# Optimization experiments

Hardware: AMD Instinct MI355X
Metric: run time of the kernel (lower is better)

## Reference

```python
import jax, jax.numpy as jnp
import numpy as np

C = 8192          # class_num == batch (required by the original per-row loop)
LS = 0.1          # label_smooth
SKIP = 3          # skip_num


def setup_inputs() -> dict:
    key = jax.random.key(0)
    preds = jax.random.normal(key, (C, C), dtype=jnp.float32)
    targets = jnp.arange(C, dtype=jnp.int32)  # row i's gt class is i, matching the loop
    return {"preds": preds, "targets": targets}


def reference(preds, targets):
    n = preds.shape[1]
    logprobs = jax.nn.log_softmax(preds, axis=1)                     # [C, C]
    onehot = jax.nn.one_hot(targets, n, dtype=jnp.float32)
    # torch.clamp(one_hot, min=LS/(C-1), max=1-LS): label smoothing
    smoothed = jnp.clip(onehot, LS / (n - 1), 1.0 - LS)

    # Per row i, skip the top SKIP classes by logprob, skipping over the gt class i.
    # Taking top (SKIP+1) always contains enough non-gt entries.
    _, topk_idx = jax.lax.top_k(logprobs, SKIP + 1)                  # [C, SKIP+1]
    rows = jnp.arange(n)[:, None]
    is_gt = topk_idx == rows                                         # gt class in top-k?
    kept = ~is_gt
    rank = jnp.cumsum(kept.astype(jnp.int32), axis=1)                # 1-based rank among non-gt
    selected = kept & (rank <= SKIP)                                 # first SKIP non-gt entries

    # Scatter selected top-k indices into a [C, C] boolean skip mask.
    skip_mask = jnp.zeros((n, n), dtype=bool).at[rows, topk_idx].max(selected)

    # Row loss: -sum over non-skipped classes of smoothed_target * logprob.
    loss = -jnp.sum(jnp.where(skip_mask, 0.0, smoothed * logprobs), axis=1)  # [C]
    return jnp.mean(loss)
```

## Files before the change

### kernel.cpp

```cpp
#include <hip/hip_runtime.h>

#define C_DIM 8192
#define BLOCK 256
#define PER_THREAD 32
#define NVEC 8

__device__ __forceinline__ bool better(float a, int ia, float b, int ib) {
    return (a > b) || (a == b && ia < ib);
}

__device__ __forceinline__ void insert4(float v[4], int id[4], float x, int j) {
    if (better(x, j, v[3], id[3])) {
        v[3] = x; id[3] = j;
        if (better(v[3], id[3], v[2], id[2])) { float tv = v[2]; int ti = id[2]; v[2] = v[3]; id[2] = id[3]; v[3] = tv; id[3] = ti; }
        if (better(v[2], id[2], v[1], id[1])) { float tv = v[1]; int ti = id[1]; v[1] = v[2]; id[1] = id[2]; v[2] = tv; id[2] = ti; }
        if (better(v[1], id[1], v[0], id[0])) { float tv = v[0]; int ti = id[0]; v[0] = v[1]; id[0] = id[1]; v[1] = tv; id[1] = ti; }
    }
}

__device__ __forceinline__ int slot2col(int tid, int s) {
    return ((s >> 2) * BLOCK + tid) * 4 + (s & 3);
}

__global__ __launch_bounds__(BLOCK) void row_loss_kernel(const float* __restrict__ preds,
                                                         const int* __restrict__ targets,
                                                         float* __restrict__ row_loss) {
    const int row  = blockIdx.x;
    const int tid  = threadIdx.x;
    const int lane = tid & 63;
    const int wid  = tid >> 6;

    const float*  base = preds + (size_t)row * C_DIM;
    const float4* rp   = (const float4*)base;

    __shared__ float s_s[4], s_l[4];
    __shared__ float s_tv[16];
    __shared__ int   s_ti[16];

    float xgt = 0.0f;
    if (tid == 0) xgt = base[targets[row]];

    float r[PER_THREAD];
    float lsum = 0.0f;
    float lv = -INFINITY;
    int   ls = 0;

#pragma unroll
    for (int v = 0; v < NVEC; ++v) {
        float4 f = rp[v * BLOCK + tid];
        float e0 = f.x, e1 = f.y, e2 = f.z, e3 = f.w;
        r[v * 4 + 0] = e0; r[v * 4 + 1] = e1; r[v * 4 + 2] = e2; r[v * 4 + 3] = e3;
        lsum += (e0 + e1) + (e2 + e3);
        if (e0 > lv) { lv = e0; ls = v * 4 + 0; }
        if (e1 > lv) { lv = e1; ls = v * 4 + 1; }
        if (e2 > lv) { lv = e2; ls = v * 4 + 2; }
        if (e3 > lv) { lv = e3; ls = v * 4 + 3; }
    }

    float wsum = lsum;
#pragma unroll
    for (int o = 32; o; o >>= 1) wsum += __shfl_xor(wsum, o);
    if (lane == 0) s_s[wid] = wsum;

    int lj = slot2col(tid, ls);
    float wtv[4]; int wti[4];
#pragma unroll
    for (int round = 0; round < 4; ++round) {
        float rv = lv; int ri = lj;
#pragma unroll
        for (int o = 32; o; o >>= 1) {
            float ov = __shfl_xor(rv, o);
            int   oi = __shfl_xor(ri, o);
            if (better(ov, oi, rv, ri)) { rv = ov; ri = oi; }
        }
        wtv[round] = rv; wti[round] = ri;
        if (lj == ri) {
            r[ls] = -INFINITY;
            lv = r[0]; ls = 0;
#pragma unroll
            for (int k = 1; k < PER_THREAD; ++k)
                if (r[k] > lv) { lv = r[k]; ls = k; }
            lj = slot2col(tid, ls);
        }
    }
    if (lane == 0) {
#pragma unroll
        for (int k = 0; k < 4; ++k) { s_tv[wid * 4 + k] = wtv[k]; s_ti[wid * 4 + k] = wti[k]; }
    }
    __syncthreads();

    const float m = fmaxf(fmaxf(s_tv[0], s_tv[4]), fmaxf(s_tv[8], s_tv[12]));

    float le = 0.0f;
#pragma unroll
    for (int k = 0; k < PER_THREAD; ++k) le += __expf(r[k] - m);
#pragma unroll
    for (int o = 32; o; o >>= 1) le += __shfl_xor(le, o);
    if (lane == 0) s_l[wid] = le;
    __syncthreads();

    if (tid == 0) {
        const float Sx = s_s[0] + s_s[1] + s_s[2] + s_s[3];
        float l = s_l[0] + s_l[1] + s_l[2] + s_l[3];
#pragma unroll
        for (int k = 0; k < 16; ++k) l += __expf(s_tv[k] - m);

        float fv[4] = { -INFINITY, -INFINITY, -INFINITY, -INFINITY };
        int   fi[4] = { 0x7FFFFFFF, 0x7FFFFFFF, 0x7FFFFFFF, 0x7FFFFFFF };
#pragma unroll
        for (int k = 0; k < 16; ++k) insert4(fv, fi, s_tv[k], s_ti[k]);

        const float logZ  = m + __logf(l);
        const float lp_gt = xgt - logZ;

        float skip_x = 0.0f; int cnt = 0;
#pragma unroll
        for (int k = 0; k < 4; ++k)
            if (fi[k] != row && cnt < 3) { skip_x += fv[k]; ++cnt; }

        const float S_lp    = Sx - (float)C_DIM * logZ;
        const float skip_lp = skip_x - 3.0f * logZ;
        const float eps     = 0.1f / (float)(C_DIM - 1);

        row_loss[row] = -(0.9f * lp_gt + eps * (S_lp - lp_gt - skip_lp));
    }
}

__global__ __launch_bounds__(BLOCK) void mean_reduce_kernel(const float* __restrict__ row_loss,
                                                            float* __restrict__ out) {
    const int tid = threadIdx.x;
    float s = 0.0f;
    for (int i = tid; i < C_DIM; i += BLOCK) s += row_loss[i];
#pragma unroll
    for (int o = 32; o; o >>= 1) s += __shfl_xor(s, o);
    __shared__ float sm[4];
    if ((tid & 63) == 0) sm[tid >> 6] = s;
    __syncthreads();
    if (tid == 0) out[0] = (sm[0] + sm[1] + sm[2] + sm[3]) / (float)C_DIM;
}

extern "C" void kernel_launch(void* const* d_in, const int* in_sizes, int n_in,
                              void* d_out, int out_size, void* d_ws, size_t ws_size,
                              hipStream_t stream) {
    const float* preds   = (const float*)d_in[0];
    const int*   targets = (const int*)d_in[1];
    float*       out     = (float*)d_out;
    float*       ws      = (float*)d_ws;

    row_loss_kernel<<<C_DIM, BLOCK, 0, stream>>>(preds, targets, ws);
    mean_reduce_kernel<<<1, BLOCK, 0, stream>>>(ws, out);
}
```

Baseline: 371.7 us.

## Fuse exp-sum into load pass, drop max-shift and second barrier, simplify top-k

Each row's sum of exponentials is now accumulated in the same pass that loads the row, without subtracting the row max first. That removes the second exp loop, its warp reduction and one block-wide barrier. The per-warp top-4 selection now finds the max with fmaxf shuffles and uses a ballot to pick the owning lane, which recovers the column, instead of shuffling value/index pairs with tie-breaking. The mean reduction switches to float4 loads. Skipping the max shift risks exp overflow for large logits, and tie handling among equal values changes.

```diff
diff --git a/kernel.cpp b/kernel.cpp
--- a/kernel.cpp
+++ b/kernel.cpp
@@ -5,21 +5,13 @@
 #define PER_THREAD 32
 #define NVEC 8
 
-__device__ __forceinline__ bool better(float a, int ia, float b, int ib) {
-    return (a > b) || (a == b && ia < ib);
-}
-
 __device__ __forceinline__ void insert4(float v[4], int id[4], float x, int j) {
-    if (better(x, j, v[3], id[3])) {
+    if (x > v[3]) {
         v[3] = x; id[3] = j;
-        if (better(v[3], id[3], v[2], id[2])) { float tv = v[2]; int ti = id[2]; v[2] = v[3]; id[2] = id[3]; v[3] = tv; id[3] = ti; }
-        if (better(v[2], id[2], v[1], id[1])) { float tv = v[1]; int ti = id[1]; v[1] = v[2]; id[1] = id[2]; v[2] = tv; id[2] = ti; }
-        if (better(v[1], id[1], v[0], id[0])) { float tv = v[0]; int ti = id[0]; v[0] = v[1]; id[0] = id[1]; v[1] = tv; id[1] = ti; }
+        if (v[3] > v[2]) { float tv = v[2]; int ti = id[2]; v[2] = v[3]; id[2] = id[3]; v[3] = tv; id[3] = ti; }
+        if (v[2] > v[1]) { float tv = v[1]; int ti = id[1]; v[1] = v[2]; id[1] = id[2]; v[2] = tv; id[2] = ti; }
+        if (v[1] > v[0]) { float tv = v[0]; int ti = id[0]; v[0] = v[1]; id[0] = id[1]; v[1] = tv; id[1] = ti; }
     }
-}
-
-__device__ __forceinline__ int slot2col(int tid, int s) {
-    return ((s >> 2) * BLOCK + tid) * 4 + (s & 3);
 }
 
 __global__ __launch_bounds__(BLOCK) void row_loss_kernel(const float* __restrict__ preds,
@@ -41,76 +33,72 @@
     if (tid == 0) xgt = base[targets[row]];
 
     float r[PER_THREAD];
-    float lsum = 0.0f;
+    float lsum = 0.0f, lexp = 0.0f;
     float lv = -INFINITY;
-    int   ls = 0;
 
 #pragma unroll
     for (int v = 0; v < NVEC; ++v) {
         float4 f = rp[v * BLOCK + tid];
-        float e0 = f.x, e1 = f.y, e2 = f.z, e3 = f.w;
-        r[v * 4 + 0] = e0; r[v * 4 + 1] = e1; r[v * 4 + 2] = e2; r[v * 4 + 3] = e3;
-        lsum += (e0 + e1) + (e2 + e3);
-        if (e0 > lv) { lv = e0; ls = v * 4 + 0; }
-        if (e1 > lv) { lv = e1; ls = v * 4 + 1; }
-        if (e2 > lv) { lv = e2; ls = v * 4 + 2; }
-        if (e3 > lv) { lv = e3; ls = v * 4 + 3; }
+        r[v * 4 + 0] = f.x; r[v * 4 + 1] = f.y; r[v * 4 + 2] = f.z; r[v * 4 + 3] = f.w;
+        lsum += (f.x + f.y) + (f.z + f.w);
+        lexp += (__expf(f.x) + __expf(f.y)) + (__expf(f.z) + __expf(f.w));
+        lv = fmaxf(fmaxf(lv, fmaxf(f.x, f.y)), fmaxf(f.z, f.w));
     }
 
-    float wsum = lsum;
+    float wsum = lsum, wexp = lexp;
 #pragma unroll
-    for (int o = 32; o; o >>= 1) wsum += __shfl_xor(wsum, o);
-    if (lane == 0) s_s[wid] = wsum;
+    for (int o = 32; o; o >>= 1) {
+        wsum += __shfl_xor(wsum, o);
+        wexp += __shfl_xor(wexp, o);
+    }
 
-    int lj = slot2col(tid, ls);
     float wtv[4]; int wti[4];
 #pragma unroll
     for (int round = 0; round < 4; ++round) {
-        float rv = lv; int ri = lj;
+        float rv = lv;
 #pragma unroll
-        for (int o = 32; o; o >>= 1) {
-            float ov = __shfl_xor(rv, o);
-            int   oi = __shfl_xor(ri, o);
-            if (better(ov, oi, rv, ri)) { rv = ov; ri = oi; }
+        for (int o = 32; o; o >>= 1) rv = fmaxf(rv, __shfl_xor(rv, o));
+        unsigned long long own = __ballot(lv == rv);
+        int owner = __ffsll((long long)own) - 1;
+        int gcol = 0;
+        if (lane == owner) {
+            bool killed = false;
+            int slot = 0;
+#pragma unroll
+            for (int k = 0; k < PER_THREAD; ++k) {
+                bool hit = (!killed) && (r[k] == rv);
+                if (hit) { slot = k; killed = true; }
+            }
+#pragma unroll
+            for (int k = 0; k < PER_THREAD; ++k)
+                if (k == slot) r[k] = -INFINITY;
+            gcol = ((slot >> 2) * BLOCK + tid) * 4 + (slot & 3);
+            lv = r[0];
+#pragma unroll
+            for (int k = 1; k < PER_THREAD; ++k) lv = fmaxf(lv, r[k]);
         }
-        wtv[round] = rv; wti[round] = ri;
-        if (lj == ri) {
-            r[ls] = -INFINITY;
-            lv = r[0]; ls = 0;
-#pragma unroll
-            for (int k = 1; k < PER_THREAD; ++k)
-                if (r[k] > lv) { lv = r[k]; ls = k; }
-            lj = slot2col(tid, ls);
-        }
+        gcol = __shfl(gcol, owner);
+        wtv[round] = rv; wti[round] = gcol;
     }
+
     if (lane == 0) {
+        s_s[wid] = wsum;
+        s_l[wid] = wexp;
 #pragma unroll
         for (int k = 0; k < 4; ++k) { s_tv[wid * 4 + k] = wtv[k]; s_ti[wid * 4 + k] = wti[k]; }
     }
     __syncthreads();
 
-    const float m = fmaxf(fmaxf(s_tv[0], s_tv[4]), fmaxf(s_tv[8], s_tv[12]));
-
-    float le = 0.0f;
-#pragma unroll
-    for (int k = 0; k < PER_THREAD; ++k) le += __expf(r[k] - m);
-#pragma unroll
-    for (int o = 32; o; o >>= 1) le += __shfl_xor(le, o);
-    if (lane == 0) s_l[wid] = le;
-    __syncthreads();
-
     if (tid == 0) {
-        const float Sx = s_s[0] + s_s[1] + s_s[2] + s_s[3];
-        float l = s_l[0] + s_l[1] + s_l[2] + s_l[3];
-#pragma unroll
-        for (int k = 0; k < 16; ++k) l += __expf(s_tv[k] - m);
+        const float Sx = (s_s[0] + s_s[1]) + (s_s[2] + s_s[3]);
+        const float l  = (s_l[0] + s_l[1]) + (s_l[2] + s_l[3]);
 
         float fv[4] = { -INFINITY, -INFINITY, -INFINITY, -INFINITY };
-        int   fi[4] = { 0x7FFFFFFF, 0x7FFFFFFF, 0x7FFFFFFF, 0x7FFFFFFF };
+        int   fi[4] = { 0, 0, 0, 0 };
 #pragma unroll
         for (int k = 0; k < 16; ++k) insert4(fv, fi, s_tv[k], s_ti[k]);
 
-        const float logZ  = m + __logf(l);
+        const float logZ  = __logf(l);
         const float lp_gt = xgt - logZ;
 
         float skip_x = 0.0f; int cnt = 0;
@@ -129,14 +117,19 @@
 __global__ __launch_bounds__(BLOCK) void mean_reduce_kernel(const float* __restrict__ row_loss,
                                                             float* __restrict__ out) {
     const int tid = threadIdx.x;
+    const float4* rl = (const float4*)row_loss;
     float s = 0.0f;
-    for (int i = tid; i < C_DIM; i += BLOCK) s += row_loss[i];
+#pragma unroll
+    for (int v = 0; v < 8; ++v) {
+        float4 f = rl[v * BLOCK + tid];
+        s += (f.x + f.y) + (f.z + f.w);
+    }
 #pragma unroll
     for (int o = 32; o; o >>= 1) s += __shfl_xor(s, o);
     __shared__ float sm[4];
     if ((tid & 63) == 0) sm[tid >> 6] = s;
     __syncthreads();
-    if (tid == 0) out[0] = (sm[0] + sm[1] + sm[2] + sm[3]) / (float)C_DIM;
+    if (tid == 0) out[0] = ((sm[0] + sm[1]) + (sm[2] + sm[3])) / (float)C_DIM;
 }
 
 extern "C" void kernel_launch(void* const* d_in, const int* in_sizes, int n_in,
```

Result: faster. 361.4 us (-2.8%).
